# Kernel optimization log

Measured on AMD Instinct MI355X. Metric: run time of the kernel, lower is better.

## Reference

```python
import jax, jax.numpy as jnp
import numpy as np

T, B, D, H = 256, 128, 512, 512


def setup_inputs() -> dict:
    key = jax.random.key(0)
    ks = jax.random.split(key, 9)
    s = 0.01  # init scale from the original module
    return {
        "X": jax.random.normal(ks[0], (T, B, D), dtype=jnp.float32),
        "Wa_x": s * jax.random.normal(ks[1], (D, H), dtype=jnp.float32),
        "Wi_x": s * jax.random.normal(ks[2], (D, H), dtype=jnp.float32),
        "Wf_x": s * jax.random.normal(ks[3], (D, H), dtype=jnp.float32),
        "Wo_x": s * jax.random.normal(ks[4], (D, H), dtype=jnp.float32),
        "Wa_h": s * jax.random.normal(ks[5], (H, H), dtype=jnp.float32),
        "Wi_h": s * jax.random.normal(ks[6], (H, H), dtype=jnp.float32),
        "Wf_h": s * jax.random.normal(ks[7], (H, H), dtype=jnp.float32),
        "Wo_h": s * jax.random.normal(ks[8], (H, H), dtype=jnp.float32),
        "ba": jnp.zeros((H,), dtype=jnp.float32),
        "bi": jnp.zeros((H,), dtype=jnp.float32),
        "bf": jnp.zeros((H,), dtype=jnp.float32),
        "bo": jnp.zeros((H,), dtype=jnp.float32),
    }


def reference(X, Wa_x, Wi_x, Wf_x, Wo_x, Wa_h, Wi_h, Wf_h, Wo_h, ba, bi, bf, bo):
    # Concatenate gate weights/biases so each step does one fused matmul per
    # source (input / hidden). Math is identical to four separate matmuls.
    Wx = jnp.concatenate([Wa_x, Wi_x, Wf_x, Wo_x], axis=1)  # [D, 4H]
    Wh = jnp.concatenate([Wa_h, Wi_h, Wf_h, Wo_h], axis=1)  # [H, 4H]
    b = jnp.concatenate([ba, bi, bf, bo], axis=0)            # [4H]
    n = ba.shape[0]

    # Precompute input projections for all timesteps in one big matmul: [T,B,4H]
    Xg = jnp.einsum('tbd,dg->tbg', X, Wx) + b

    def step(carry, xg):
        h_prev, s_prev = carry
        g = xg + h_prev @ Wh  # note: t=0 uses h_prev=0, matching the original
        a = jnp.tanh(g[:, 0 * n:1 * n])
        i = jax.nn.sigmoid(g[:, 1 * n:2 * n])
        f = jax.nn.sigmoid(g[:, 2 * n:3 * n])
        o = jax.nn.sigmoid(g[:, 3 * n:4 * n])
        s = a * i + s_prev * f  # t=0: s_prev=0 -> s = a*i, matching original
        h = jnp.tanh(s) * o
        return (h, s), h

    h0 = jnp.zeros((X.shape[1], n), dtype=X.dtype)
    s0 = jnp.zeros((X.shape[1], n), dtype=X.dtype)
    _, outputs = jax.lax.scan(step, (h0, s0), Xg)  # [T, B, H]
    return outputs
```

## Files before the change

### kernel.cpp

```cpp
#include <hip/hip_runtime.h>


#define TT 256
#define BB 128
#define DD 512
#define HH 512
#define KK 1024
#define NBLK 256

typedef __bf16 bf16x8 __attribute__((ext_vector_type(8)));
typedef float f32x4 __attribute__((ext_vector_type(4)));
typedef unsigned short u16x8 __attribute__((ext_vector_type(8)));
typedef unsigned long long u64;

union h128 { u64 q[2]; bf16x8 v; };

__device__ __forceinline__ unsigned short f2bf(float f) {
  unsigned b = __builtin_bit_cast(unsigned, f);
  return (unsigned short)((b + 0x7fffu + ((b >> 16) & 1u)) >> 16);
}
__device__ __forceinline__ float fexp(float x) {
  return __builtin_amdgcn_exp2f(x * 1.4426950408889634f);
}
__device__ __forceinline__ float fsig(float x) {
  return __builtin_amdgcn_rcpf(1.0f + fexp(-x));
}
__device__ __forceinline__ float ftanh(float x) {
  return 2.0f * fsig(2.0f * x) - 1.0f;
}

__global__ __launch_bounds__(256) void convert_x_kernel(const float* __restrict__ X,
                                                        unsigned short* __restrict__ Xbf) {
  size_t i = (size_t)blockIdx.x * 256 + threadIdx.x;
  const float4* src = (const float4*)X + i * 2;
  float4 v0 = src[0], v1 = src[1];
  u16x8 o;
  o[0] = f2bf(v0.x); o[1] = f2bf(v0.y); o[2] = f2bf(v0.z); o[3] = f2bf(v0.w);
  o[4] = f2bf(v1.x); o[5] = f2bf(v1.y); o[6] = f2bf(v1.z); o[7] = f2bf(v1.w);
  ((u16x8*)Xbf)[i] = o;
}

__global__ __launch_bounds__(256) void build_wt_kernel(
    const float* __restrict__ Wax, const float* __restrict__ Wix,
    const float* __restrict__ Wfx, const float* __restrict__ Wox,
    const float* __restrict__ Wah, const float* __restrict__ Wih,
    const float* __restrict__ Wfh, const float* __restrict__ Woh,
    unsigned short* __restrict__ WT) {
  __shared__ float tile[64][65];
  int bid = blockIdx.x;
  int q  = bid >> 7;
  int jt = (bid >> 4) & 7;
  int kt = bid & 15;
  const float* Wx[4] = {Wax, Wix, Wfx, Wox};
  const float* Wh[4] = {Wah, Wih, Wfh, Woh};
  const float* src = (kt < 8) ? Wx[q] : Wh[q];
  int k0 = (kt & 7) * 64;
  int j0 = jt * 64;
  int tid = threadIdx.x;
#pragma unroll
  for (int e = 0; e < 16; ++e) {
    int lin = e * 256 + tid;
    int kk = lin >> 6, jj = lin & 63;
    tile[kk][jj] = src[(size_t)(k0 + kk) * HH + j0 + jj];
  }
  __syncthreads();
#pragma unroll
  for (int e = 0; e < 16; ++e) {
    int lin = e * 256 + tid;
    int jj = lin >> 6, kk = lin & 63;
    WT[(size_t)(q * HH + j0 + jj) * KK + kt * 64 + kk] = f2bf(tile[kk][jj]);
  }
}

__global__ __launch_bounds__(256, 1) void lstm_main(
    const unsigned short* __restrict__ Xbf,
    const unsigned short* __restrict__ WT,
    const float* __restrict__ ba, const float* __restrict__ bi,
    const float* __restrict__ bfg, const float* __restrict__ bo,
    unsigned short* __restrict__ hbq,
    float* __restrict__ out,
    unsigned* __restrict__ cnt) {
  const int tid  = threadIdx.x;
  const int bid  = blockIdx.x;
  const int lane = tid & 63;
  const int wave = tid >> 6;
  const int rb = bid >> 5;
  const int cb = bid & 31;
  const int l15 = lane & 15;
  const int lk8 = (lane >> 4) * 8;
  const int rbase = rb * 16;
  const int colg = cb * 16 + l15;
  const int wk = wave * 128;

  bf16x8 wf[4][8];
#pragma unroll
  for (int g = 0; g < 4; ++g) {
    const unsigned short* wg = WT + (size_t)(g * HH + colg) * KK + lk8;
#pragma unroll
    for (int c = 0; c < 8; ++c) {
      int kb = (c < 4) ? (wk + c * 32) : (DD + wk + (c - 4) * 32);
      wf[g][c] = *(const bf16x8*)(wg + kb);
    }
  }

  const int el_row = tid >> 4;
  const int el_col = tid & 15;
  const int el_colg = cb * 16 + el_col;
  const int el_rowg = rbase + el_row;
  const float b0 = ba[el_colg], b1 = bi[el_colg], b2 = bfg[el_colg], b3 = bo[el_colg];
  const int lsrc = (el_row >> 2) * 16 + el_col;
  const int rsrc = el_row & 3;

  const unsigned short* xbase = Xbf + (size_t)(rbase + l15) * DD + wk + lk8;
  const size_t ostore_el = (size_t)el_rowg * HH + el_colg;

  unsigned short* hgrp = hbq + (size_t)rb * (2 * 8192);
  size_t hload_off[4];
#pragma unroll
  for (int c = 0; c < 4; ++c) {
    int j0 = wk + c * 32 + lk8;
    hload_off[c] = (size_t)(j0 >> 4) * 256 + (size_t)l15 * 16 + (j0 & 15);
  }
  const size_t hstore_off = (size_t)cb * 256 + (size_t)el_row * 16 + el_col;

  __shared__ f32x4 part[2][4][4][64];

  float s_c = 0.f;

  for (int t = 0; t < TT; ++t) {
    const unsigned short* xt = xbase + (size_t)t * BB * DD;
    bf16x8 ax0 = *(const bf16x8*)(xt);
    bf16x8 ax1 = *(const bf16x8*)(xt + 32);
    bf16x8 ax2 = *(const bf16x8*)(xt + 64);
    bf16x8 ax3 = *(const bf16x8*)(xt + 96);

    f32x4 acc[4];
#pragma unroll
    for (int g = 0; g < 4; ++g) {
      f32x4 z = {0.f, 0.f, 0.f, 0.f};
      acc[g] = __builtin_amdgcn_mfma_f32_16x16x32_bf16(ax0, wf[g][0], z, 0, 0, 0);
      acc[g] = __builtin_amdgcn_mfma_f32_16x16x32_bf16(ax1, wf[g][1], acc[g], 0, 0, 0);
      acc[g] = __builtin_amdgcn_mfma_f32_16x16x32_bf16(ax2, wf[g][2], acc[g], 0, 0, 0);
      acc[g] = __builtin_amdgcn_mfma_f32_16x16x32_bf16(ax3, wf[g][3], acc[g], 0, 0, 0);
    }

    if (t > 0) {
      const unsigned* cptr = cnt + (size_t)(rb * TT + (t - 1)) * 16;
      unsigned v = __hip_atomic_load(cptr, __ATOMIC_RELAXED, __HIP_MEMORY_SCOPE_AGENT);
      while (v < 32u) {
        __builtin_amdgcn_s_sleep(1);
        v = __hip_atomic_load(cptr, __ATOMIC_RELAXED, __HIP_MEMORY_SCOPE_AGENT);
      }
      asm volatile("" ::: "memory");

      const unsigned short* hp = hgrp + (size_t)(((t & 1) ^ 1)) * 8192;
      h128 u0, u1, u2, u3;
      const u64* q0 = (const u64*)(hp + hload_off[0]);
      const u64* q1 = (const u64*)(hp + hload_off[1]);
      const u64* q2 = (const u64*)(hp + hload_off[2]);
      const u64* q3 = (const u64*)(hp + hload_off[3]);
      u0.q[0] = __hip_atomic_load(q0,     __ATOMIC_RELAXED, __HIP_MEMORY_SCOPE_AGENT);
      u0.q[1] = __hip_atomic_load(q0 + 1, __ATOMIC_RELAXED, __HIP_MEMORY_SCOPE_AGENT);
      u1.q[0] = __hip_atomic_load(q1,     __ATOMIC_RELAXED, __HIP_MEMORY_SCOPE_AGENT);
      u1.q[1] = __hip_atomic_load(q1 + 1, __ATOMIC_RELAXED, __HIP_MEMORY_SCOPE_AGENT);
      u2.q[0] = __hip_atomic_load(q2,     __ATOMIC_RELAXED, __HIP_MEMORY_SCOPE_AGENT);
      u2.q[1] = __hip_atomic_load(q2 + 1, __ATOMIC_RELAXED, __HIP_MEMORY_SCOPE_AGENT);
      u3.q[0] = __hip_atomic_load(q3,     __ATOMIC_RELAXED, __HIP_MEMORY_SCOPE_AGENT);
      u3.q[1] = __hip_atomic_load(q3 + 1, __ATOMIC_RELAXED, __HIP_MEMORY_SCOPE_AGENT);

#pragma unroll
      for (int g = 0; g < 4; ++g) {
        acc[g] = __builtin_amdgcn_mfma_f32_16x16x32_bf16(u0.v, wf[g][4], acc[g], 0, 0, 0);
        acc[g] = __builtin_amdgcn_mfma_f32_16x16x32_bf16(u1.v, wf[g][5], acc[g], 0, 0, 0);
        acc[g] = __builtin_amdgcn_mfma_f32_16x16x32_bf16(u2.v, wf[g][6], acc[g], 0, 0, 0);
        acc[g] = __builtin_amdgcn_mfma_f32_16x16x32_bf16(u3.v, wf[g][7], acc[g], 0, 0, 0);
      }
    }

    const int pb = t & 1;
#pragma unroll
    for (int g = 0; g < 4; ++g) part[pb][wave][g][lane] = acc[g];
    __syncthreads();

    float g0 = b0, g1 = b1, g2 = b2, g3 = b3;
#pragma unroll
    for (int w = 0; w < 4; ++w) {
      g0 += ((const float*)&part[pb][w][0][lsrc])[rsrc];
      g1 += ((const float*)&part[pb][w][1][lsrc])[rsrc];
      g2 += ((const float*)&part[pb][w][2][lsrc])[rsrc];
      g3 += ((const float*)&part[pb][w][3][lsrc])[rsrc];
    }
    float av = ftanh(g0);
    float iv = fsig(g1);
    float fv = fsig(g2);
    float ov = fsig(g3);
    s_c = av * iv + s_c * fv;
    float hv = ftanh(s_c) * ov;

    if (t < TT - 1) {
      unsigned mybf = (unsigned)f2bf(hv);
      unsigned nxbf = (unsigned)__shfl_down((int)mybf, 1);
      if ((tid & 1) == 0) {
        unsigned pack = mybf | (nxbf << 16);
        unsigned* dst = (unsigned*)(hgrp + (size_t)pb * 8192 + hstore_off);
        __hip_atomic_store(dst, pack, __ATOMIC_RELAXED, __HIP_MEMORY_SCOPE_AGENT);
      }
      __syncthreads();
      if (tid == 0)
        __hip_atomic_fetch_add(cnt + (size_t)(rb * TT + t) * 16, 1u,
                               __ATOMIC_RELAXED, __HIP_MEMORY_SCOPE_AGENT);
    }

    out[(size_t)t * BB * HH + ostore_el] = hv;

#pragma unroll
    for (int g = 0; g < 4; ++g)
#pragma unroll
      for (int c = 4; c < 8; ++c)
        asm volatile("" : "+v"(wf[g][c]));
  }
}

extern "C" void kernel_launch(void* const* d_in, const int* in_sizes, int n_in,
                              void* d_out, int out_size, void* d_ws, size_t ws_size,
                              hipStream_t stream) {
  const float* X   = (const float*)d_in[0];
  const float* Wax = (const float*)d_in[1];
  const float* Wix = (const float*)d_in[2];
  const float* Wfx = (const float*)d_in[3];
  const float* Wox = (const float*)d_in[4];
  const float* Wah = (const float*)d_in[5];
  const float* Wih = (const float*)d_in[6];
  const float* Wfh = (const float*)d_in[7];
  const float* Woh = (const float*)d_in[8];
  const float* ba  = (const float*)d_in[9];
  const float* bi  = (const float*)d_in[10];
  const float* bf  = (const float*)d_in[11];
  const float* bo  = (const float*)d_in[12];
  float* out = (float*)d_out;

  char* ws = (char*)d_ws;
  unsigned short* Xbf = (unsigned short*)ws;
  unsigned short* WT  = (unsigned short*)(ws + 33554432);
  unsigned short* hbq = (unsigned short*)(ws + 33554432 + 4194304);
  unsigned* cnt = (unsigned*)(ws + 33554432 + 4194304 + 262144);

  hipMemsetAsync(cnt, 0, 131072, stream);

  convert_x_kernel<<<8192, 256, 0, stream>>>(X, Xbf);
  build_wt_kernel<<<512, 256, 0, stream>>>(Wax, Wix, Wfx, Wox, Wah, Wih, Wfh, Woh, WT);
  lstm_main<<<NBLK, 256, 0, stream>>>(Xbf, WT, ba, bi, bf, bo, hbq, out, cnt);
}
```

Baseline: 644.1 us.

## Process two batch row-blocks per workgroup to halve persistent block count

Halves the grid from 256 to 128 persistent workgroups, so each block handles two 16-row batch chunks in sequence within every timestep and reuses the same register-resident weight fragments for both. The aim is fewer blocks taking part in the cross-block counter synchronisation and less grid-wide contention, with the serial work inside each block doubled in exchange. The two chunks are interleaved so one chunk's input projection and wait can overlap the other's publish, but each timestep's critical path inside a block gets longer.

```diff
diff --git a/kernel.cpp b/kernel.cpp
--- a/kernel.cpp
+++ b/kernel.cpp
@@ -6,7 +6,7 @@
 #define DD 512
 #define HH 512
 #define KK 1024
-#define NBLK 256
+#define NBLK 128
 
 typedef __bf16 bf16x8 __attribute__((ext_vector_type(8)));
 typedef float f32x4 __attribute__((ext_vector_type(4)));
@@ -84,11 +84,10 @@
   const int bid  = blockIdx.x;
   const int lane = tid & 63;
   const int wave = tid >> 6;
-  const int rb = bid >> 5;
+  const int pg = bid >> 5;
   const int cb = bid & 31;
   const int l15 = lane & 15;
   const int lk8 = (lane >> 4) * 8;
-  const int rbase = rb * 16;
   const int colg = cb * 16 + l15;
   const int wk = wave * 128;
 
@@ -106,15 +105,23 @@
   const int el_row = tid >> 4;
   const int el_col = tid & 15;
   const int el_colg = cb * 16 + el_col;
-  const int el_rowg = rbase + el_row;
   const float b0 = ba[el_colg], b1 = bi[el_colg], b2 = bfg[el_colg], b3 = bo[el_colg];
   const int lsrc = (el_row >> 2) * 16 + el_col;
   const int rsrc = el_row & 3;
 
-  const unsigned short* xbase = Xbf + (size_t)(rbase + l15) * DD + wk + lk8;
-  const size_t ostore_el = (size_t)el_rowg * HH + el_colg;
-
-  unsigned short* hgrp = hbq + (size_t)rb * (2 * 8192);
+  const unsigned short* xbase[2];
+  unsigned short* hgrp[2];
+  size_t ostore_el[2];
+  unsigned* cbase[2];
+#pragma unroll
+  for (int ch = 0; ch < 2; ++ch) {
+    const int rb = pg * 2 + ch;
+    const int rbase = rb * 16;
+    xbase[ch] = Xbf + (size_t)(rbase + l15) * DD + wk + lk8;
+    hgrp[ch] = hbq + (size_t)rb * (2 * 8192);
+    ostore_el[ch] = (size_t)(rbase + el_row) * HH + el_colg;
+    cbase[ch] = cnt + (size_t)(rb * TT) * 16;
+  }
   size_t hload_off[4];
 #pragma unroll
   for (int c = 0; c < 4; ++c) {
@@ -123,95 +130,98 @@
   }
   const size_t hstore_off = (size_t)cb * 256 + (size_t)el_row * 16 + el_col;
 
-  __shared__ f32x4 part[2][4][4][64];
-
-  float s_c = 0.f;
+  __shared__ f32x4 part[2][2][4][4][64];
+
+  float s_c[2] = {0.f, 0.f};
 
   for (int t = 0; t < TT; ++t) {
-    const unsigned short* xt = xbase + (size_t)t * BB * DD;
-    bf16x8 ax0 = *(const bf16x8*)(xt);
-    bf16x8 ax1 = *(const bf16x8*)(xt + 32);
-    bf16x8 ax2 = *(const bf16x8*)(xt + 64);
-    bf16x8 ax3 = *(const bf16x8*)(xt + 96);
-
-    f32x4 acc[4];
-#pragma unroll
-    for (int g = 0; g < 4; ++g) {
-      f32x4 z = {0.f, 0.f, 0.f, 0.f};
-      acc[g] = __builtin_amdgcn_mfma_f32_16x16x32_bf16(ax0, wf[g][0], z, 0, 0, 0);
-      acc[g] = __builtin_amdgcn_mfma_f32_16x16x32_bf16(ax1, wf[g][1], acc[g], 0, 0, 0);
-      acc[g] = __builtin_amdgcn_mfma_f32_16x16x32_bf16(ax2, wf[g][2], acc[g], 0, 0, 0);
-      acc[g] = __builtin_amdgcn_mfma_f32_16x16x32_bf16(ax3, wf[g][3], acc[g], 0, 0, 0);
+#pragma unroll
+    for (int ch = 0; ch < 2; ++ch) {
+      const unsigned short* xt = xbase[ch] + (size_t)t * BB * DD;
+      bf16x8 ax0 = *(const bf16x8*)(xt);
+      bf16x8 ax1 = *(const bf16x8*)(xt + 32);
+      bf16x8 ax2 = *(const bf16x8*)(xt + 64);
+      bf16x8 ax3 = *(const bf16x8*)(xt + 96);
+
+      f32x4 acc[4];
+#pragma unroll
+      for (int g = 0; g < 4; ++g) {
+        f32x4 z = {0.f, 0.f, 0.f, 0.f};
+        acc[g] = __builtin_amdgcn_mfma_f32_16x16x32_bf16(ax0, wf[g][0], z, 0, 0, 0);
+        acc[g] = __builtin_amdgcn_mfma_f32_16x16x32_bf16(ax1, wf[g][1], acc[g], 0, 0, 0);
+        acc[g] = __builtin_amdgcn_mfma_f32_16x16x32_bf16(ax2, wf[g][2], acc[g], 0, 0, 0);
+        acc[g] = __builtin_amdgcn_mfma_f32_16x16x32_bf16(ax3, wf[g][3], acc[g], 0, 0, 0);
+      }
+
+      if (t > 0) {
+        const unsigned* cptr = cbase[ch] + (size_t)(t - 1) * 16;
+        unsigned v = __hip_atomic_load(cptr, __ATOMIC_RELAXED, __HIP_MEMORY_SCOPE_AGENT);
+        while (v < 32u) {
+          __builtin_amdgcn_s_sleep(1);
+          v = __hip_atomic_load(cptr, __ATOMIC_RELAXED, __HIP_MEMORY_SCOPE_AGENT);
+        }
+        asm volatile("" ::: "memory");
+
+        const unsigned short* hp = hgrp[ch] + (size_t)(((t & 1) ^ 1)) * 8192;
+        h128 u0, u1, u2, u3;
+        const u64* q0 = (const u64*)(hp + hload_off[0]);
+        const u64* q1 = (const u64*)(hp + hload_off[1]);
+        const u64* q2 = (const u64*)(hp + hload_off[2]);
+        const u64* q3 = (const u64*)(hp + hload_off[3]);
+        u0.q[0] = __hip_atomic_load(q0,     __ATOMIC_RELAXED, __HIP_MEMORY_SCOPE_AGENT);
+        u0.q[1] = __hip_atomic_load(q0 + 1, __ATOMIC_RELAXED, __HIP_MEMORY_SCOPE_AGENT);
+        u1.q[0] = __hip_atomic_load(q1,     __ATOMIC_RELAXED, __HIP_MEMORY_SCOPE_AGENT);
+        u1.q[1] = __hip_atomic_load(q1 + 1, __ATOMIC_RELAXED, __HIP_MEMORY_SCOPE_AGENT);
+        u2.q[0] = __hip_atomic_load(q2,     __ATOMIC_RELAXED, __HIP_MEMORY_SCOPE_AGENT);
+        u2.q[1] = __hip_atomic_load(q2 + 1, __ATOMIC_RELAXED, __HIP_MEMORY_SCOPE_AGENT);
+        u3.q[0] = __hip_atomic_load(q3,     __ATOMIC_RELAXED, __HIP_MEMORY_SCOPE_AGENT);
+        u3.q[1] = __hip_atomic_load(q3 + 1, __ATOMIC_RELAXED, __HIP_MEMORY_SCOPE_AGENT);
+
+#pragma unroll
+        for (int g = 0; g < 4; ++g) {
+          acc[g] = __builtin_amdgcn_mfma_f32_16x16x32_bf16(u0.v, wf[g][4], acc[g], 0, 0, 0);
+          acc[g] = __builtin_amdgcn_mfma_f32_16x16x32_bf16(u1.v, wf[g][5], acc[g], 0, 0, 0);
+          acc[g] = __builtin_amdgcn_mfma_f32_16x16x32_bf16(u2.v, wf[g][6], acc[g], 0, 0, 0);
+          acc[g] = __builtin_amdgcn_mfma_f32_16x16x32_bf16(u3.v, wf[g][7], acc[g], 0, 0, 0);
+        }
+      }
+
+      const int pb = t & 1;
+#pragma unroll
+      for (int g = 0; g < 4; ++g) part[ch][pb][wave][g][lane] = acc[g];
+      __syncthreads();
+
+      float g0 = b0, g1 = b1, g2 = b2, g3 = b3;
+#pragma unroll
+      for (int w = 0; w < 4; ++w) {
+        g0 += ((const float*)&part[ch][pb][w][0][lsrc])[rsrc];
+        g1 += ((const float*)&part[ch][pb][w][1][lsrc])[rsrc];
+        g2 += ((const float*)&part[ch][pb][w][2][lsrc])[rsrc];
+        g3 += ((const float*)&part[ch][pb][w][3][lsrc])[rsrc];
+      }
+      float av = ftanh(g0);
+      float iv = fsig(g1);
+      float fv = fsig(g2);
+      float ov = fsig(g3);
+      s_c[ch] = av * iv + s_c[ch] * fv;
+      float hv = ftanh(s_c[ch]) * ov;
+
+      if (t < TT - 1) {
+        unsigned mybf = (unsigned)f2bf(hv);
+        unsigned nxbf = (unsigned)__shfl_down((int)mybf, 1);
+        if ((tid & 1) == 0) {
+          unsigned pack = mybf | (nxbf << 16);
+          unsigned* dst = (unsigned*)(hgrp[ch] + (size_t)pb * 8192 + hstore_off);
+          __hip_atomic_store(dst, pack, __ATOMIC_RELAXED, __HIP_MEMORY_SCOPE_AGENT);
+        }
+        __syncthreads();
+        if (tid == 0)
+          __hip_atomic_fetch_add(cbase[ch] + (size_t)t * 16, 1u,
+                                 __ATOMIC_RELAXED, __HIP_MEMORY_SCOPE_AGENT);
+      }
+
+      out[(size_t)t * BB * HH + ostore_el[ch]] = hv;
     }
-
-    if (t > 0) {
-      const unsigned* cptr = cnt + (size_t)(rb * TT + (t - 1)) * 16;
-      unsigned v = __hip_atomic_load(cptr, __ATOMIC_RELAXED, __HIP_MEMORY_SCOPE_AGENT);
-      while (v < 32u) {
-        __builtin_amdgcn_s_sleep(1);
-        v = __hip_atomic_load(cptr, __ATOMIC_RELAXED, __HIP_MEMORY_SCOPE_AGENT);
-      }
-      asm volatile("" ::: "memory");
-
-      const unsigned short* hp = hgrp + (size_t)(((t & 1) ^ 1)) * 8192;
-      h128 u0, u1, u2, u3;
-      const u64* q0 = (const u64*)(hp + hload_off[0]);
-      const u64* q1 = (const u64*)(hp + hload_off[1]);
-      const u64* q2 = (const u64*)(hp + hload_off[2]);
-      const u64* q3 = (const u64*)(hp + hload_off[3]);
-      u0.q[0] = __hip_atomic_load(q0,     __ATOMIC_RELAXED, __HIP_MEMORY_SCOPE_AGENT);
-      u0.q[1] = __hip_atomic_load(q0 + 1, __ATOMIC_RELAXED, __HIP_MEMORY_SCOPE_AGENT);
-      u1.q[0] = __hip_atomic_load(q1,     __ATOMIC_RELAXED, __HIP_MEMORY_SCOPE_AGENT);
-      u1.q[1] = __hip_atomic_load(q1 + 1, __ATOMIC_RELAXED, __HIP_MEMORY_SCOPE_AGENT);
-      u2.q[0] = __hip_atomic_load(q2,     __ATOMIC_RELAXED, __HIP_MEMORY_SCOPE_AGENT);
-      u2.q[1] = __hip_atomic_load(q2 + 1, __ATOMIC_RELAXED, __HIP_MEMORY_SCOPE_AGENT);
-      u3.q[0] = __hip_atomic_load(q3,     __ATOMIC_RELAXED, __HIP_MEMORY_SCOPE_AGENT);
-      u3.q[1] = __hip_atomic_load(q3 + 1, __ATOMIC_RELAXED, __HIP_MEMORY_SCOPE_AGENT);
-
-#pragma unroll
-      for (int g = 0; g < 4; ++g) {
-        acc[g] = __builtin_amdgcn_mfma_f32_16x16x32_bf16(u0.v, wf[g][4], acc[g], 0, 0, 0);
-        acc[g] = __builtin_amdgcn_mfma_f32_16x16x32_bf16(u1.v, wf[g][5], acc[g], 0, 0, 0);
-        acc[g] = __builtin_amdgcn_mfma_f32_16x16x32_bf16(u2.v, wf[g][6], acc[g], 0, 0, 0);
-        acc[g] = __builtin_amdgcn_mfma_f32_16x16x32_bf16(u3.v, wf[g][7], acc[g], 0, 0, 0);
-      }
-    }
-
-    const int pb = t & 1;
-#pragma unroll
-    for (int g = 0; g < 4; ++g) part[pb][wave][g][lane] = acc[g];
-    __syncthreads();
-
-    float g0 = b0, g1 = b1, g2 = b2, g3 = b3;
-#pragma unroll
-    for (int w = 0; w < 4; ++w) {
-      g0 += ((const float*)&part[pb][w][0][lsrc])[rsrc];
-      g1 += ((const float*)&part[pb][w][1][lsrc])[rsrc];
-      g2 += ((const float*)&part[pb][w][2][lsrc])[rsrc];
-      g3 += ((const float*)&part[pb][w][3][lsrc])[rsrc];
-    }
-    float av = ftanh(g0);
-    float iv = fsig(g1);
-    float fv = fsig(g2);
-    float ov = fsig(g3);
-    s_c = av * iv + s_c * fv;
-    float hv = ftanh(s_c) * ov;
-
-    if (t < TT - 1) {
-      unsigned mybf = (unsigned)f2bf(hv);
-      unsigned nxbf = (unsigned)__shfl_down((int)mybf, 1);
-      if ((tid & 1) == 0) {
-        unsigned pack = mybf | (nxbf << 16);
-        unsigned* dst = (unsigned*)(hgrp + (size_t)pb * 8192 + hstore_off);
-        __hip_atomic_store(dst, pack, __ATOMIC_RELAXED, __HIP_MEMORY_SCOPE_AGENT);
-      }
-      __syncthreads();
-      if (tid == 0)
-        __hip_atomic_fetch_add(cnt + (size_t)(rb * TT + t) * 16, 1u,
-                               __ATOMIC_RELAXED, __HIP_MEMORY_SCOPE_AGENT);
-    }
-
-    out[(size_t)t * BB * HH + ostore_el] = hv;
 
 #pragma unroll
     for (int g = 0; g < 4; ++g)
```

New measurement: 1.112 ms. 1.73x slower.

## Replace per-step counter barrier with poison-flag polling on per-timestep h buffers

Applied to the files above, without the earlier changes.

Drops the per-block atomic counter and the extra __syncthreads before signaling. Each timestep now gets its own hidden-state buffer that is pre-filled with 0xFF, and consumers spin directly on the data until no word equals the poison value. This removes one synchronization round trip per step, a counter increment plus a separate poll. In exchange it needs a much larger workspace (about 33MB) and a big memset before every launch, and it relies on a bf16 pair never packing to 0xFFFFFFFF.

```diff
diff --git a/kernel.cpp b/kernel.cpp
--- a/kernel.cpp
+++ b/kernel.cpp
@@ -7,13 +7,11 @@
 #define HH 512
 #define KK 1024
 #define NBLK 256
+#define POISON 0xFFFFFFFFu
 
 typedef __bf16 bf16x8 __attribute__((ext_vector_type(8)));
 typedef float f32x4 __attribute__((ext_vector_type(4)));
 typedef unsigned short u16x8 __attribute__((ext_vector_type(8)));
-typedef unsigned long long u64;
-
-union h128 { u64 q[2]; bf16x8 v; };
 
 __device__ __forceinline__ unsigned short f2bf(float f) {
   unsigned b = __builtin_bit_cast(unsigned, f);
@@ -77,9 +75,8 @@
     const unsigned short* __restrict__ WT,
     const float* __restrict__ ba, const float* __restrict__ bi,
     const float* __restrict__ bfg, const float* __restrict__ bo,
-    unsigned short* __restrict__ hbq,
-    float* __restrict__ out,
-    unsigned* __restrict__ cnt) {
+    unsigned* __restrict__ hbq,
+    float* __restrict__ out) {
   const int tid  = threadIdx.x;
   const int bid  = blockIdx.x;
   const int lane = tid & 63;
@@ -114,14 +111,14 @@
   const unsigned short* xbase = Xbf + (size_t)(rbase + l15) * DD + wk + lk8;
   const size_t ostore_el = (size_t)el_rowg * HH + el_colg;
 
-  unsigned short* hgrp = hbq + (size_t)rb * (2 * 8192);
-  size_t hload_off[4];
+  unsigned hload_off[4];
 #pragma unroll
   for (int c = 0; c < 4; ++c) {
     int j0 = wk + c * 32 + lk8;
-    hload_off[c] = (size_t)(j0 >> 4) * 256 + (size_t)l15 * 16 + (j0 & 15);
-  }
-  const size_t hstore_off = (size_t)cb * 256 + (size_t)el_row * 16 + el_col;
+    hload_off[c] = (unsigned)((j0 >> 4) * 128 + l15 * 8 + ((j0 & 15) >> 1));
+  }
+  const unsigned hstore_off = (unsigned)(cb * 128 + el_row * 8 + (el_col >> 1));
+  unsigned* hgrp = hbq + (size_t)rb * 4096;
 
   __shared__ f32x4 part[2][4][4][64];
 
@@ -145,35 +142,48 @@
     }
 
     if (t > 0) {
-      const unsigned* cptr = cnt + (size_t)(rb * TT + (t - 1)) * 16;
-      unsigned v = __hip_atomic_load(cptr, __ATOMIC_RELAXED, __HIP_MEMORY_SCOPE_AGENT);
-      while (v < 32u) {
+      const unsigned* hp = hgrp + (size_t)(t - 1) * 32768;
+      uint4 q0, q1, q2, q3;
+      while (true) {
+        const uint4* p0 = (const uint4*)(hp + hload_off[0]);
+        const uint4* p1 = (const uint4*)(hp + hload_off[1]);
+        const uint4* p2 = (const uint4*)(hp + hload_off[2]);
+        const uint4* p3 = (const uint4*)(hp + hload_off[3]);
+        q0.x = __hip_atomic_load((const unsigned*)p0 + 0, __ATOMIC_RELAXED, __HIP_MEMORY_SCOPE_AGENT);
+        q0.y = __hip_atomic_load((const unsigned*)p0 + 1, __ATOMIC_RELAXED, __HIP_MEMORY_SCOPE_AGENT);
+        q0.z = __hip_atomic_load((const unsigned*)p0 + 2, __ATOMIC_RELAXED, __HIP_MEMORY_SCOPE_AGENT);
+        q0.w = __hip_atomic_load((const unsigned*)p0 + 3, __ATOMIC_RELAXED, __HIP_MEMORY_SCOPE_AGENT);
+        q1.x = __hip_atomic_load((const unsigned*)p1 + 0, __ATOMIC_RELAXED, __HIP_MEMORY_SCOPE_AGENT);
+        q1.y = __hip_atomic_load((const unsigned*)p1 + 1, __ATOMIC_RELAXED, __HIP_MEMORY_SCOPE_AGENT);
+        q1.z = __hip_atomic_load((const unsigned*)p1 + 2, __ATOMIC_RELAXED, __HIP_MEMORY_SCOPE_AGENT);
+        q1.w = __hip_atomic_load((const unsigned*)p1 + 3, __ATOMIC_RELAXED, __HIP_MEMORY_SCOPE_AGENT);
+        q2.x = __hip_atomic_load((const unsigned*)p2 + 0, __ATOMIC_RELAXED, __HIP_MEMORY_SCOPE_AGENT);
+        q2.y = __hip_atomic_load((const unsigned*)p2 + 1, __ATOMIC_RELAXED, __HIP_MEMORY_SCOPE_AGENT);
+        q2.z = __hip_atomic_load((const unsigned*)p2 + 2, __ATOMIC_RELAXED, __HIP_MEMORY_SCOPE_AGENT);
+        q2.w = __hip_atomic_load((const unsigned*)p2 + 3, __ATOMIC_RELAXED, __HIP_MEMORY_SCOPE_AGENT);
+        q3.x = __hip_atomic_load((const unsigned*)p3 + 0, __ATOMIC_RELAXED, __HIP_MEMORY_SCOPE_AGENT);
+        q3.y = __hip_atomic_load((const unsigned*)p3 + 1, __ATOMIC_RELAXED, __HIP_MEMORY_SCOPE_AGENT);
+        q3.z = __hip_atomic_load((const unsigned*)p3 + 2, __ATOMIC_RELAXED, __HIP_MEMORY_SCOPE_AGENT);
+        q3.w = __hip_atomic_load((const unsigned*)p3 + 3, __ATOMIC_RELAXED, __HIP_MEMORY_SCOPE_AGENT);
+        unsigned ok = 1u;
+        ok &= (q0.x != POISON) & (q0.y != POISON) & (q0.z != POISON) & (q0.w != POISON);
+        ok &= (q1.x != POISON) & (q1.y != POISON) & (q1.z != POISON) & (q1.w != POISON);
+        ok &= (q2.x != POISON) & (q2.y != POISON) & (q2.z != POISON) & (q2.w != POISON);
+        ok &= (q3.x != POISON) & (q3.y != POISON) & (q3.z != POISON) & (q3.w != POISON);
+        if (__all(ok != 0u)) break;
         __builtin_amdgcn_s_sleep(1);
-        v = __hip_atomic_load(cptr, __ATOMIC_RELAXED, __HIP_MEMORY_SCOPE_AGENT);
       }
-      asm volatile("" ::: "memory");
-
-      const unsigned short* hp = hgrp + (size_t)(((t & 1) ^ 1)) * 8192;
-      h128 u0, u1, u2, u3;
-      const u64* q0 = (const u64*)(hp + hload_off[0]);
-      const u64* q1 = (const u64*)(hp + hload_off[1]);
-      const u64* q2 = (const u64*)(hp + hload_off[2]);
-      const u64* q3 = (const u64*)(hp + hload_off[3]);
-      u0.q[0] = __hip_atomic_load(q0,     __ATOMIC_RELAXED, __HIP_MEMORY_SCOPE_AGENT);
-      u0.q[1] = __hip_atomic_load(q0 + 1, __ATOMIC_RELAXED, __HIP_MEMORY_SCOPE_AGENT);
-      u1.q[0] = __hip_atomic_load(q1,     __ATOMIC_RELAXED, __HIP_MEMORY_SCOPE_AGENT);
-      u1.q[1] = __hip_atomic_load(q1 + 1, __ATOMIC_RELAXED, __HIP_MEMORY_SCOPE_AGENT);
-      u2.q[0] = __hip_atomic_load(q2,     __ATOMIC_RELAXED, __HIP_MEMORY_SCOPE_AGENT);
-      u2.q[1] = __hip_atomic_load(q2 + 1, __ATOMIC_RELAXED, __HIP_MEMORY_SCOPE_AGENT);
-      u3.q[0] = __hip_atomic_load(q3,     __ATOMIC_RELAXED, __HIP_MEMORY_SCOPE_AGENT);
-      u3.q[1] = __hip_atomic_load(q3 + 1, __ATOMIC_RELAXED, __HIP_MEMORY_SCOPE_AGENT);
+      bf16x8 hf0 = __builtin_bit_cast(bf16x8, q0);
+      bf16x8 hf1 = __builtin_bit_cast(bf16x8, q1);
+      bf16x8 hf2 = __builtin_bit_cast(bf16x8, q2);
+      bf16x8 hf3 = __builtin_bit_cast(bf16x8, q3);
 
 #pragma unroll
       for (int g = 0; g < 4; ++g) {
-        acc[g] = __builtin_amdgcn_mfma_f32_16x16x32_bf16(u0.v, wf[g][4], acc[g], 0, 0, 0);
-        acc[g] = __builtin_amdgcn_mfma_f32_16x16x32_bf16(u1.v, wf[g][5], acc[g], 0, 0, 0);
-        acc[g] = __builtin_amdgcn_mfma_f32_16x16x32_bf16(u2.v, wf[g][6], acc[g], 0, 0, 0);
-        acc[g] = __builtin_amdgcn_mfma_f32_16x16x32_bf16(u3.v, wf[g][7], acc[g], 0, 0, 0);
+        acc[g] = __builtin_amdgcn_mfma_f32_16x16x32_bf16(hf0, wf[g][4], acc[g], 0, 0, 0);
+        acc[g] = __builtin_amdgcn_mfma_f32_16x16x32_bf16(hf1, wf[g][5], acc[g], 0, 0, 0);
+        acc[g] = __builtin_amdgcn_mfma_f32_16x16x32_bf16(hf2, wf[g][6], acc[g], 0, 0, 0);
+        acc[g] = __builtin_amdgcn_mfma_f32_16x16x32_bf16(hf3, wf[g][7], acc[g], 0, 0, 0);
       }
     }
 
@@ -202,13 +212,9 @@
       unsigned nxbf = (unsigned)__shfl_down((int)mybf, 1);
       if ((tid & 1) == 0) {
         unsigned pack = mybf | (nxbf << 16);
-        unsigned* dst = (unsigned*)(hgrp + (size_t)pb * 8192 + hstore_off);
+        unsigned* dst = hgrp + (size_t)t * 32768 + hstore_off;
         __hip_atomic_store(dst, pack, __ATOMIC_RELAXED, __HIP_MEMORY_SCOPE_AGENT);
       }
-      __syncthreads();
-      if (tid == 0)
-        __hip_atomic_fetch_add(cnt + (size_t)(rb * TT + t) * 16, 1u,
-                               __ATOMIC_RELAXED, __HIP_MEMORY_SCOPE_AGENT);
     }
 
     out[(size_t)t * BB * HH + ostore_el] = hv;
@@ -242,12 +248,11 @@
   char* ws = (char*)d_ws;
   unsigned short* Xbf = (unsigned short*)ws;
   unsigned short* WT  = (unsigned short*)(ws + 33554432);
-  unsigned short* hbq = (unsigned short*)(ws + 33554432 + 4194304);
-  unsigned* cnt = (unsigned*)(ws + 33554432 + 4194304 + 262144);
-
-  hipMemsetAsync(cnt, 0, 131072, stream);
+  unsigned* hbq = (unsigned*)(ws + 33554432 + 4194304);
+
+  hipMemsetAsync(hbq, 0xFF, (size_t)(TT - 1) * 32768 * 4, stream);
 
   convert_x_kernel<<<8192, 256, 0, stream>>>(X, Xbf);
   build_wt_kernel<<<512, 256, 0, stream>>>(Wax, Wix, Wfx, Wox, Wah, Wih, Wfh, Woh, WT);
-  lstm_main<<<NBLK, 256, 0, stream>>>(Xbf, WT, ba, bi, bf, bo, hbq, out, cnt);
-}
+  lstm_main<<<NBLK, 256, 0, stream>>>(Xbf, WT, ba, bi, bf, bo, hbq, out);
+}
```

New measurement: 883.9 us. +37.2%, slower.
